# Kernel tuning notes

Measured on AMD Instinct MI355X. Metric: run time of the kernel, lower is better.

## Reference

```python
import jax, jax.numpy as jnp
import numpy as np

B, R, N, D_IN, D_OUT = 8, 8, 1024, 256, 256


def setup_inputs() -> dict:
    key = jax.random.key(0)
    k1, k2, k3, k4 = jax.random.split(key, 4)
    x = jax.random.normal(k1, (B, N, D_IN), dtype=jnp.float32)
    adj_stack = jax.random.uniform(k2, (B, R, N, N), dtype=jnp.float32)
    # per-relation Linear params, stacked: W[r] maps D_IN -> D_OUT
    bound = 1.0 / np.sqrt(D_IN)
    W = jax.random.uniform(k3, (R, D_IN, D_OUT), minval=-bound, maxval=bound, dtype=jnp.float32)
    b = jax.random.uniform(k4, (R, D_OUT), minval=-bound, maxval=bound, dtype=jnp.float32)
    return {"x": x, "adj_stack": adj_stack, "W": W, "b": b}


def reference(x, adj_stack, W, b):
    # support[b,r,n,e] = x[b,n,:] @ W[r] + b[r]
    support = jnp.einsum('bnd,rde->brne', x, W) + b[None, :, None, :]
    # out[b,m,e] = sum_r adj[b,r,m,:] @ support[b,r,:,e]
    out = jnp.einsum('brmn,brne->bme', adj_stack, support)
    return jax.nn.relu(out)
```

## Files before the change

### kernel.cpp

```cpp
#include <hip/hip_runtime.h>
#include <hip/hip_bf16.h>


#define Rr 8
#define Nn 1024
#define Dd 256
#define AP 264
#define EPF 68
#define EPS 72

typedef __attribute__((ext_vector_type(8))) short short8;
typedef __attribute__((ext_vector_type(4))) float f32x4;

__device__ __forceinline__ short f2bf(float f) {
    unsigned u = __builtin_bit_cast(unsigned, f);
    u += 0x7fffu + ((u >> 16) & 1u);
    return (short)(u >> 16);
}

__device__ __forceinline__ short8 cvt8(f32x4 lo, f32x4 hi) {
    short8 t;
    t[0] = f2bf(lo[0]); t[1] = f2bf(lo[1]); t[2] = f2bf(lo[2]); t[3] = f2bf(lo[3]);
    t[4] = f2bf(hi[0]); t[5] = f2bf(hi[1]); t[6] = f2bf(hi[2]); t[7] = f2bf(hi[3]);
    return t;
}

__global__ void prep_w_kernel(const float* __restrict__ W, short* __restrict__ Wt) {
    __shared__ short T[64][72];
    const int tid = threadIdx.x;
    const int et = blockIdx.x, dt = blockIdx.y, r = blockIdx.z;
    const float* Wr = W + ((size_t)r * Dd + dt * 64) * Dd + et * 64;
    #pragma unroll
    for (int i = 0; i < 4; ++i) {
        int idx = tid + i * 256;
        int d_l = idx >> 4;
        int e4  = (idx & 15) * 4;
        f32x4 v = *(const f32x4*)(Wr + d_l * Dd + e4);
        T[e4 + 0][d_l] = f2bf(v[0]);
        T[e4 + 1][d_l] = f2bf(v[1]);
        T[e4 + 2][d_l] = f2bf(v[2]);
        T[e4 + 3][d_l] = f2bf(v[3]);
    }
    __syncthreads();
    short* o = Wt + ((size_t)r * Dd + et * 64) * Dd + dt * 64;
    #pragma unroll
    for (int i = 0; i < 2; ++i) {
        int idx = tid + i * 256;
        *(short8*)(o + (idx >> 3) * Dd + (idx & 7) * 8) = *(const short8*)&T[idx >> 3][(idx & 7) * 8];
    }
}

__global__ __launch_bounds__(256, 2) void support_kernel(
        const float* __restrict__ x, const short* __restrict__ Wt,
        const float* __restrict__ bias, short* __restrict__ sup) {
    __shared__ short As[64 * AP];
    __shared__ short Bs[64 * AP];

    const int tid = threadIdx.x;
    const int wave = tid >> 6, lane = tid & 63;
    const int quad = lane >> 4, l16 = lane & 15;
    const int bid = blockIdx.x;
    const int b   = bid & 7;
    const int e_t = (bid >> 3) & 3;
    const int n_t = (bid >> 5) & 15;
    const int r   = bid >> 9;
    const int e0 = e_t * 64, n0 = n_t * 64;
    const int we = wave & 1, wn = wave >> 1;

    const short* wp = Wt + ((size_t)r * Dd + e0) * Dd;
    const float* xb = x + ((size_t)b * Nn + n0) * Dd;

    #pragma unroll
    for (int p = 0; p < 8; ++p) {
        int idx = tid + p * 256;
        int row = idx >> 5, c = idx & 31;
        *(short8*)&As[row * AP + c * 8] = *(const short8*)(wp + row * Dd + c * 8);
    }
    #pragma unroll
    for (int p = 0; p < 8; ++p) {
        int idx = tid + p * 256;
        int row = idx >> 5, c = idx & 31;
        const float* pp = xb + row * Dd + c * 8;
        *(short8*)&Bs[row * AP + c * 8] = cvt8(*(const f32x4*)pp, *(const f32x4*)(pp + 4));
    }
    __syncthreads();

    f32x4 acc[2][2] = {};
    #pragma unroll
    for (int kk = 0; kk < 8; ++kk) {
        short8 a[2], bb[2];
        #pragma unroll
        for (int i = 0; i < 2; ++i)
            a[i] = *(const short8*)&As[(we * 32 + i * 16 + l16) * AP + kk * 32 + quad * 8];
        #pragma unroll
        for (int j = 0; j < 2; ++j)
            bb[j] = *(const short8*)&Bs[(wn * 32 + j * 16 + l16) * AP + kk * 32 + quad * 8];
        #pragma unroll
        for (int i = 0; i < 2; ++i)
            #pragma unroll
            for (int j = 0; j < 2; ++j)
                acc[i][j] = __builtin_amdgcn_mfma_f32_16x16x32_bf16(a[i], bb[j], acc[i][j], 0, 0, 0);
    }

    __syncthreads();
    short* E = As;
    #pragma unroll
    for (int i = 0; i < 2; ++i)
        #pragma unroll
        for (int reg = 0; reg < 4; ++reg) {
            int row = we * 32 + i * 16 + quad * 4 + reg;
            float bv = bias[r * Dd + e0 + row];
            #pragma unroll
            for (int j = 0; j < 2; ++j)
                E[row * EPS + wn * 32 + j * 16 + l16] = f2bf(acc[i][j][reg] + bv);
        }
    __syncthreads();
    #pragma unroll
    for (int p = 0; p < 2; ++p) {
        int idx = tid + p * 256;
        int row = idx >> 3, c = idx & 7;
        *(short8*)(sup + (((size_t)((b * Rr + r) * Dd + e0 + row)) << 10) + n0 + c * 8) =
            *(const short8*)&E[row * EPS + c * 8];
    }
}

__global__ __launch_bounds__(256, 2) void gcn_gemm_kernel(
        const float* __restrict__ adj, const short* __restrict__ sup,
        float* __restrict__ out) {
    __shared__ short As[64 * AP];
    __shared__ short Bs[64 * AP];

    const int tid = threadIdx.x;
    const int wave = tid >> 6, lane = tid & 63;
    const int quad = lane >> 4, l16 = lane & 15;
    const int bid = blockIdx.x;
    const int b   = bid & 7;
    const int e_t = (bid >> 3) & 3;
    const int m_t = bid >> 5;
    const int e0 = e_t * 64, m0 = m_t * 64;
    const int wm = wave & 1, we = wave >> 1;

    f32x4 axv[16];
    short8 sv[8];

    auto gload = [&](int rr, int ks) {
        const float* ap = adj + ((size_t)(b * Rr + rr) * Nn + m0) * Nn + ks;
        const short* bp = sup + (((size_t)((b * Rr + rr) * Dd + e0)) << 10) + ks;
        #pragma unroll
        for (int p = 0; p < 8; ++p) {
            int idx = tid + p * 256;
            int row = idx >> 5, c = idx & 31;
            const float* pp = ap + (size_t)row * Nn + c * 8;
            axv[2 * p]     = *(const f32x4*)pp;
            axv[2 * p + 1] = *(const f32x4*)(pp + 4);
            sv[p] = *(const short8*)(bp + ((size_t)row << 10) + c * 8);
        }
    };
    auto stage = [&]() {
        #pragma unroll
        for (int p = 0; p < 8; ++p) {
            int idx = tid + p * 256;
            int row = idx >> 5, c = idx & 31;
            *(short8*)&As[row * AP + c * 8] = cvt8(axv[2 * p], axv[2 * p + 1]);
            *(short8*)&Bs[row * AP + c * 8] = sv[p];
        }
    };

    f32x4 acc[2][2] = {};
    gload(0, 0);
    for (int st = 0; st < 32; ++st) {
        stage();
        __syncthreads();
        if (st < 31) gload((st + 1) >> 2, ((st + 1) & 3) * 256);
        #pragma unroll
        for (int kk = 0; kk < 8; ++kk) {
            short8 a[2], bb[2];
            #pragma unroll
            for (int i = 0; i < 2; ++i)
                a[i] = *(const short8*)&As[(wm * 32 + i * 16 + l16) * AP + kk * 32 + quad * 8];
            #pragma unroll
            for (int j = 0; j < 2; ++j)
                bb[j] = *(const short8*)&Bs[(we * 32 + j * 16 + l16) * AP + kk * 32 + quad * 8];
            #pragma unroll
            for (int i = 0; i < 2; ++i)
                #pragma unroll
                for (int j = 0; j < 2; ++j)
                    acc[i][j] = __builtin_amdgcn_mfma_f32_16x16x32_bf16(a[i], bb[j], acc[i][j], 0, 0, 0);
        }
        __syncthreads();
    }

    float* E = (float*)As;
    #pragma unroll
    for (int i = 0; i < 2; ++i)
        #pragma unroll
        for (int reg = 0; reg < 4; ++reg) {
            int row = wm * 32 + i * 16 + quad * 4 + reg;
            #pragma unroll
            for (int j = 0; j < 2; ++j)
                E[row * EPF + we * 32 + j * 16 + l16] = fmaxf(acc[i][j][reg], 0.f);
        }
    __syncthreads();
    #pragma unroll
    for (int p = 0; p < 4; ++p) {
        int idx = tid + p * 256;
        int row = idx >> 4, c = idx & 15;
        *(f32x4*)(out + ((size_t)(b * Nn + m0 + row)) * Dd + e0 + c * 4) =
            *(const f32x4*)&E[row * EPF + c * 4];
    }
}

extern "C" void kernel_launch(void* const* d_in, const int* in_sizes, int n_in,
                              void* d_out, int out_size, void* d_ws, size_t ws_size,
                              hipStream_t stream) {
    const float* x    = (const float*)d_in[0];
    const float* adj  = (const float*)d_in[1];
    const float* W    = (const float*)d_in[2];
    const float* bias = (const float*)d_in[3];
    float* out = (float*)d_out;
    short* sup = (short*)d_ws;
    short* Wt  = (short*)((char*)d_ws + (32u << 20));

    prep_w_kernel<<<dim3(4, 4, 8), 256, 0, stream>>>(W, Wt);
    support_kernel<<<4096, 256, 0, stream>>>(x, Wt, bias, sup);
    gcn_gemm_kernel<<<512, 256, 0, stream>>>(adj, sup, out);
}
```

Measured before the change: 450.0 us.

## Pipeline both GEMMs with double-buffered 64-wide K tiles and explicit waitcnt

Both the support and aggregation kernels now move K in 64-wide slices through double-buffered LDS, with two register sets of prefetched global data. Manual vmcnt/lgkmcnt waits and raw barriers let global loads for step t+3 overlap MFMA work on the current buffer, and s_setprio raises priority during MFMA issue. The smaller LDS footprint allows three blocks per CU, and the gcn block index is remapped so neighbouring blocks land on different XCDs. The cost is more barriers per K step and fragile hand-counted wait values.

```diff
diff --git a/kernel.cpp b/kernel.cpp
--- a/kernel.cpp
+++ b/kernel.cpp
@@ -1,11 +1,10 @@
 #include <hip/hip_runtime.h>
-#include <hip/hip_bf16.h>
 
 
 #define Rr 8
 #define Nn 1024
 #define Dd 256
-#define AP 264
+#define SP 104
 #define EPF 68
 #define EPS 72
 
@@ -50,69 +49,97 @@
     }
 }
 
-__global__ __launch_bounds__(256, 2) void support_kernel(
+__global__ __launch_bounds__(256, 3) void support_kernel(
         const float* __restrict__ x, const short* __restrict__ Wt,
         const float* __restrict__ bias, short* __restrict__ sup) {
-    __shared__ short As[64 * AP];
-    __shared__ short Bs[64 * AP];
+    __shared__ short As[2][64 * SP];
+    __shared__ short Bs[2][64 * SP];
 
     const int tid = threadIdx.x;
     const int wave = tid >> 6, lane = tid & 63;
     const int quad = lane >> 4, l16 = lane & 15;
-    const int bid = blockIdx.x;
-    const int b   = bid & 7;
-    const int e_t = (bid >> 3) & 3;
-    const int n_t = (bid >> 5) & 15;
-    const int r   = bid >> 9;
+    const int lrow = tid >> 3, lc = tid & 7;
+    const int d = blockIdx.x;
+    const int b = d & 7, rest = d >> 3;
+    const int e_t = rest & 3, n_t = (rest >> 2) & 15, r = rest >> 6;
     const int e0 = e_t * 64, n0 = n_t * 64;
     const int we = wave & 1, wn = wave >> 1;
 
     const short* wp = Wt + ((size_t)r * Dd + e0) * Dd;
     const float* xb = x + ((size_t)b * Nn + n0) * Dd;
 
-    #pragma unroll
-    for (int p = 0; p < 8; ++p) {
-        int idx = tid + p * 256;
-        int row = idx >> 5, c = idx & 31;
-        *(short8*)&As[row * AP + c * 8] = *(const short8*)(wp + row * Dd + c * 8);
-    }
-    #pragma unroll
-    for (int p = 0; p < 8; ++p) {
-        int idx = tid + p * 256;
-        int row = idx >> 5, c = idx & 31;
-        const float* pp = xb + row * Dd + c * 8;
-        *(short8*)&Bs[row * AP + c * 8] = cvt8(*(const f32x4*)pp, *(const f32x4*)(pp + 4));
-    }
-    __syncthreads();
+    short8 Wa0[2], Wa1[2];
+    f32x4  Xv0[4], Xv1[4];
+
+#define SGLOAD(WW, XX, t) do { int d0_ = (t) * 64;                              \
+        _Pragma("unroll")                                                       \
+        for (int p_ = 0; p_ < 2; ++p_) { int row_ = lrow + p_ * 32;             \
+            WW[p_] = *(const short8*)(wp + (size_t)row_ * Dd + d0_ + lc * 8);   \
+            const float* px_ = xb + (size_t)row_ * Dd + d0_ + lc * 8;           \
+            XX[2 * p_]     = *(const f32x4*)px_;                                \
+            XX[2 * p_ + 1] = *(const f32x4*)(px_ + 4); } } while (0)
+
+#define SWRITE(BW, WW, XX) do {                                                 \
+        _Pragma("unroll")                                                       \
+        for (int p_ = 0; p_ < 2; ++p_) { int row_ = lrow + p_ * 32;             \
+            *(short8*)&As[BW][row_ * SP + lc * 8] = WW[p_];                     \
+            *(short8*)&Bs[BW][row_ * SP + lc * 8] = cvt8(XX[2 * p_], XX[2 * p_ + 1]); } } while (0)
+
+#define SCOMP(BR) do {                                                          \
+        _Pragma("unroll")                                                       \
+        for (int kk_ = 0; kk_ < 2; ++kk_) { short8 af_[2], bf_[2];              \
+            _Pragma("unroll")                                                   \
+            for (int i_ = 0; i_ < 2; ++i_)                                      \
+                af_[i_] = *(const short8*)&As[BR][(we * 32 + i_ * 16 + l16) * SP + kk_ * 32 + quad * 8]; \
+            _Pragma("unroll")                                                   \
+            for (int j_ = 0; j_ < 2; ++j_)                                      \
+                bf_[j_] = *(const short8*)&Bs[BR][(wn * 32 + j_ * 16 + l16) * SP + kk_ * 32 + quad * 8]; \
+            __builtin_amdgcn_s_setprio(1);                                      \
+            _Pragma("unroll")                                                   \
+            for (int i_ = 0; i_ < 2; ++i_)                                      \
+                _Pragma("unroll")                                               \
+                for (int j_ = 0; j_ < 2; ++j_)                                  \
+                    acc[i_][j_] = __builtin_amdgcn_mfma_f32_16x16x32_bf16(af_[i_], bf_[j_], acc[i_][j_], 0, 0, 0); \
+            __builtin_amdgcn_s_setprio(0); } } while (0)
+
+#define SITER(t, VM, BW, WW, XX, BR) do {                                       \
+        asm volatile("s_waitcnt vmcnt(" #VM ")" ::: "memory");                  \
+        asm volatile("s_waitcnt lgkmcnt(0)" ::: "memory");                      \
+        __builtin_amdgcn_s_barrier();                                           \
+        asm volatile("" ::: "memory");                                          \
+        SWRITE(BW, WW, XX);                                                     \
+        if ((t) + 3 < 4) SGLOAD(WW, XX, (t) + 3);                               \
+        SCOMP(BR); } while (0)
 
     f32x4 acc[2][2] = {};
-    #pragma unroll
-    for (int kk = 0; kk < 8; ++kk) {
-        short8 a[2], bb[2];
-        #pragma unroll
-        for (int i = 0; i < 2; ++i)
-            a[i] = *(const short8*)&As[(we * 32 + i * 16 + l16) * AP + kk * 32 + quad * 8];
-        #pragma unroll
-        for (int j = 0; j < 2; ++j)
-            bb[j] = *(const short8*)&Bs[(wn * 32 + j * 16 + l16) * AP + kk * 32 + quad * 8];
-        #pragma unroll
-        for (int i = 0; i < 2; ++i)
-            #pragma unroll
-            for (int j = 0; j < 2; ++j)
-                acc[i][j] = __builtin_amdgcn_mfma_f32_16x16x32_bf16(a[i], bb[j], acc[i][j], 0, 0, 0);
-    }
-
-    __syncthreads();
-    short* E = As;
+    SGLOAD(Wa0, Xv0, 0);
+    SGLOAD(Wa1, Xv1, 1);
+    asm volatile("s_waitcnt vmcnt(6)" ::: "memory");
+    SWRITE(0, Wa0, Xv0);
+    SGLOAD(Wa0, Xv0, 2);
+    SITER(0, 6, 1, Wa1, Xv1, 0);
+    SITER(1, 6, 0, Wa0, Xv0, 1);
+    SITER(2, 0, 1, Wa1, Xv1, 0);
+    asm volatile("s_waitcnt lgkmcnt(0)" ::: "memory");
+    __builtin_amdgcn_s_barrier();
+    asm volatile("" ::: "memory");
+    SCOMP(1);
+#undef SGLOAD
+#undef SWRITE
+#undef SCOMP
+#undef SITER
+
+    __syncthreads();
+    short* E = &As[0][0];
     #pragma unroll
     for (int i = 0; i < 2; ++i)
         #pragma unroll
         for (int reg = 0; reg < 4; ++reg) {
-            int row = we * 32 + i * 16 + quad * 4 + reg;
-            float bv = bias[r * Dd + e0 + row];
+            int e_l = we * 32 + i * 16 + quad * 4 + reg;
+            float bv = bias[r * Dd + e0 + e_l];
             #pragma unroll
             for (int j = 0; j < 2; ++j)
-                E[row * EPS + wn * 32 + j * 16 + l16] = f2bf(acc[i][j][reg] + bv);
+                E[e_l * EPS + wn * 32 + j * 16 + l16] = f2bf(acc[i][j][reg] + bv);
         }
     __syncthreads();
     #pragma unroll
@@ -124,81 +151,98 @@
     }
 }
 
-__global__ __launch_bounds__(256, 2) void gcn_gemm_kernel(
+__global__ __launch_bounds__(256, 3) void gcn_gemm_kernel(
         const float* __restrict__ adj, const short* __restrict__ sup,
         float* __restrict__ out) {
-    __shared__ short As[64 * AP];
-    __shared__ short Bs[64 * AP];
+    __shared__ short As[2][64 * SP];
+    __shared__ short Bs[2][64 * SP];
 
     const int tid = threadIdx.x;
     const int wave = tid >> 6, lane = tid & 63;
     const int quad = lane >> 4, l16 = lane & 15;
-    const int bid = blockIdx.x;
-    const int b   = bid & 7;
-    const int e_t = (bid >> 3) & 3;
-    const int m_t = bid >> 5;
-    const int e0 = e_t * 64, m0 = m_t * 64;
+    const int lrow = tid >> 3, lc = tid & 7;
+    const int d = blockIdx.x;
+    const int L = (d & 7) * 64 + (d >> 3);
+    const int e_t = L & 3, mrow = L >> 2;
+    const int b = mrow >> 4;
+    const int m0 = (mrow & 15) * 64, e0 = e_t * 64;
     const int wm = wave & 1, we = wave >> 1;
 
-    f32x4 axv[16];
-    short8 sv[8];
-
-    auto gload = [&](int rr, int ks) {
-        const float* ap = adj + ((size_t)(b * Rr + rr) * Nn + m0) * Nn + ks;
-        const short* bp = sup + (((size_t)((b * Rr + rr) * Dd + e0)) << 10) + ks;
-        #pragma unroll
-        for (int p = 0; p < 8; ++p) {
-            int idx = tid + p * 256;
-            int row = idx >> 5, c = idx & 31;
-            const float* pp = ap + (size_t)row * Nn + c * 8;
-            axv[2 * p]     = *(const f32x4*)pp;
-            axv[2 * p + 1] = *(const f32x4*)(pp + 4);
-            sv[p] = *(const short8*)(bp + ((size_t)row << 10) + c * 8);
-        }
-    };
-    auto stage = [&]() {
-        #pragma unroll
-        for (int p = 0; p < 8; ++p) {
-            int idx = tid + p * 256;
-            int row = idx >> 5, c = idx & 31;
-            *(short8*)&As[row * AP + c * 8] = cvt8(axv[2 * p], axv[2 * p + 1]);
-            *(short8*)&Bs[row * AP + c * 8] = sv[p];
-        }
-    };
+    f32x4  Aa0[4], Aa1[4];
+    short8 Sv0[2], Sv1[2];
+
+#define GGLOAD(AA, SS, t) do { int r_ = (t) >> 4, n0_ = ((t) & 15) * 64;        \
+        const float* ap_ = adj + ((size_t)((b * Rr + r_) * Nn + m0)) * Nn + n0_; \
+        const short* sp_ = sup + (((size_t)((b * Rr + r_) * Dd + e0)) << 10) + n0_; \
+        _Pragma("unroll")                                                       \
+        for (int p_ = 0; p_ < 2; ++p_) { int row_ = lrow + p_ * 32;             \
+            const float* pa_ = ap_ + (size_t)row_ * Nn + lc * 8;                \
+            AA[2 * p_]     = *(const f32x4*)pa_;                                \
+            AA[2 * p_ + 1] = *(const f32x4*)(pa_ + 4);                          \
+            SS[p_] = *(const short8*)(sp_ + ((size_t)row_ << 10) + lc * 8); } } while (0)
+
+#define GWRITE(BW, AA, SS) do {                                                 \
+        _Pragma("unroll")                                                       \
+        for (int p_ = 0; p_ < 2; ++p_) { int row_ = lrow + p_ * 32;             \
+            *(short8*)&As[BW][row_ * SP + lc * 8] = cvt8(AA[2 * p_], AA[2 * p_ + 1]); \
+            *(short8*)&Bs[BW][row_ * SP + lc * 8] = SS[p_]; } } while (0)
+
+#define GCOMP(BR) do {                                                          \
+        _Pragma("unroll")                                                       \
+        for (int kk_ = 0; kk_ < 2; ++kk_) { short8 af_[2], bf_[2];              \
+            _Pragma("unroll")                                                   \
+            for (int i_ = 0; i_ < 2; ++i_)                                      \
+                af_[i_] = *(const short8*)&As[BR][(wm * 32 + i_ * 16 + l16) * SP + kk_ * 32 + quad * 8]; \
+            _Pragma("unroll")                                                   \
+            for (int j_ = 0; j_ < 2; ++j_)                                      \
+                bf_[j_] = *(const short8*)&Bs[BR][(we * 32 + j_ * 16 + l16) * SP + kk_ * 32 + quad * 8]; \
+            __builtin_amdgcn_s_setprio(1);                                      \
+            _Pragma("unroll")                                                   \
+            for (int i_ = 0; i_ < 2; ++i_)                                      \
+                _Pragma("unroll")                                               \
+                for (int j_ = 0; j_ < 2; ++j_)                                  \
+                    acc[i_][j_] = __builtin_amdgcn_mfma_f32_16x16x32_bf16(af_[i_], bf_[j_], acc[i_][j_], 0, 0, 0); \
+            __builtin_amdgcn_s_setprio(0); } } while (0)
+
+#define GITER(t, VM, BW, AA, SS, BR) do {                                       \
+        asm volatile("s_waitcnt vmcnt(" #VM ")" ::: "memory");                  \
+        asm volatile("s_waitcnt lgkmcnt(0)" ::: "memory");                      \
+        __builtin_amdgcn_s_barrier();                                           \
+        asm volatile("" ::: "memory");                                          \
+        GWRITE(BW, AA, SS);                                                     \
+        if ((t) + 3 < 128) GGLOAD(AA, SS, (t) + 3);                             \
+        GCOMP(BR); } while (0)
 
     f32x4 acc[2][2] = {};
-    gload(0, 0);
-    for (int st = 0; st < 32; ++st) {
-        stage();
-        __syncthreads();
-        if (st < 31) gload((st + 1) >> 2, ((st + 1) & 3) * 256);
-        #pragma unroll
-        for (int kk = 0; kk < 8; ++kk) {
-            short8 a[2], bb[2];
-            #pragma unroll
-            for (int i = 0; i < 2; ++i)
-                a[i] = *(const short8*)&As[(wm * 32 + i * 16 + l16) * AP + kk * 32 + quad * 8];
-            #pragma unroll
-            for (int j = 0; j < 2; ++j)
-                bb[j] = *(const short8*)&Bs[(we * 32 + j * 16 + l16) * AP + kk * 32 + quad * 8];
-            #pragma unroll
-            for (int i = 0; i < 2; ++i)
-                #pragma unroll
-                for (int j = 0; j < 2; ++j)
-                    acc[i][j] = __builtin_amdgcn_mfma_f32_16x16x32_bf16(a[i], bb[j], acc[i][j], 0, 0, 0);
-        }
-        __syncthreads();
-    }
-
-    float* E = (float*)As;
+    GGLOAD(Aa0, Sv0, 0);
+    GGLOAD(Aa1, Sv1, 1);
+    asm volatile("s_waitcnt vmcnt(6)" ::: "memory");
+    GWRITE(0, Aa0, Sv0);
+    GGLOAD(Aa0, Sv0, 2);
+    for (int t = 0; t < 126; t += 2) {
+        GITER(t,     6, 1, Aa1, Sv1, 0);
+        GITER(t + 1, 6, 0, Aa0, Sv0, 1);
+    }
+    GITER(126, 0, 1, Aa1, Sv1, 0);
+    asm volatile("s_waitcnt lgkmcnt(0)" ::: "memory");
+    __builtin_amdgcn_s_barrier();
+    asm volatile("" ::: "memory");
+    GCOMP(1);
+#undef GGLOAD
+#undef GWRITE
+#undef GCOMP
+#undef GITER
+
+    __syncthreads();
+    float* E = (float*)&As[0][0];
     #pragma unroll
     for (int i = 0; i < 2; ++i)
         #pragma unroll
         for (int reg = 0; reg < 4; ++reg) {
-            int row = wm * 32 + i * 16 + quad * 4 + reg;
+            int m_l = wm * 32 + i * 16 + quad * 4 + reg;
             #pragma unroll
             for (int j = 0; j < 2; ++j)
-                E[row * EPF + we * 32 + j * 16 + l16] = fmaxf(acc[i][j][reg], 0.f);
+                E[m_l * EPF + we * 32 + j * 16 + l16] = fmaxf(acc[i][j][reg], 0.f);
         }
     __syncthreads();
     #pragma unroll
```

Result: no change. 442.3 us (-1.7%).
